# Optimization experiments

Hardware: AMD Instinct MI355X
Metric: run time of the kernel (lower is better)

The kernel has to match this reference:

```python
import jax, jax.numpy as jnp
import numpy as np

D_MODEL = 1024
N_HEAD = 16
DK = D_MODEL // N_HEAD
NEG = -10000.0  # module uses masked_fill with -10000.0, not -inf


def setup_inputs() -> dict:
    key = jax.random.key(0)
    k1, k2, k3 = jax.random.split(key, 3)
    B, T = 8, 1024
    x = jax.random.normal(k1, (B, T, D_MODEL), dtype=jnp.float32)
    # torch Linear(d, 3d, bias=False): y = x @ W.T with W [3d, d]; store transposed
    w_qkv = jax.random.normal(k2, (D_MODEL, 3 * D_MODEL), dtype=jnp.float32) * (1.0 / np.sqrt(D_MODEL))
    w_proj = jax.random.normal(k3, (D_MODEL, D_MODEL), dtype=jnp.float32) * (1.0 / np.sqrt(D_MODEL))
    return {"x": x, "w_qkv": w_qkv, "w_proj": w_proj}


def reference(x, w_qkv, w_proj):
    B, T, C = x.shape
    qkv = x @ w_qkv  # [B, T, 3C]
    q, k, v = jnp.split(qkv, 3, axis=-1)
    # [B, H, T, dk]
    q = q.reshape(B, T, N_HEAD, DK).transpose(0, 2, 1, 3)
    k = k.reshape(B, T, N_HEAD, DK).transpose(0, 2, 1, 3)
    v = v.reshape(B, T, N_HEAD, DK).transpose(0, 2, 1, 3)
    att = jnp.einsum('bhqd,bhkd->bhqk', q, k) / jnp.sqrt(jnp.float32(DK))
    causal = jnp.tril(jnp.ones((T, T), dtype=bool))  # [T, T]
    att = jnp.where(causal[None, None], att, NEG)
    att = jax.nn.softmax(att, axis=-1)
    y = jnp.einsum('bhqk,bhkd->bhqd', att, v)  # [B, H, T, dk]
    y = y.transpose(0, 2, 1, 3).reshape(B, T, C)
    return y @ w_proj
```

## Files before the change

kernel.cpp:

```cpp
#include <hip/hip_runtime.h>

typedef short bf16x8 __attribute__((ext_vector_type(8)));
typedef float f32x4 __attribute__((ext_vector_type(4)));

__device__ __forceinline__ unsigned short f2bf(float f) {
  unsigned u = __builtin_bit_cast(unsigned, f);
  u += 0x7fff + ((u >> 16) & 1);
  return (unsigned short)(u >> 16);
}

__device__ __forceinline__ void gload_lds16(const void* g, void* l) {
  __builtin_amdgcn_global_load_lds(
      (const __attribute__((address_space(1))) void*)g,
      (__attribute__((address_space(3))) void*)l, 16, 0, 0);
}

__global__ __launch_bounds__(256) void cvt_f32_bf16(const float* __restrict__ in,
                                                    unsigned short* __restrict__ out,
                                                    int n4) {
  int i = blockIdx.x * blockDim.x + threadIdx.x;
  int stride = gridDim.x * blockDim.x;
  for (; i < n4; i += stride) {
    float4 v = ((const float4*)in)[i];
    ushort4 o;
    o.x = f2bf(v.x); o.y = f2bf(v.y); o.z = f2bf(v.z); o.w = f2bf(v.w);
    ((ushort4*)out)[i] = o;
  }
}

__global__ __launch_bounds__(256) void tconv(const float* __restrict__ in,
                                             unsigned short* __restrict__ out,
                                             int R, int C) {
  __shared__ float tile[32][33];
  const int c0 = blockIdx.x * 32, r0 = blockIdx.y * 32;
  const int tid = threadIdx.x;
  const int tr = tid >> 3;
  const int tc4 = tid & 7;
  float4 v = *(const float4*)&in[(size_t)(r0 + tr) * C + c0 + tc4 * 4];
  tile[tr][tc4 * 4 + 0] = v.x;
  tile[tr][tc4 * 4 + 1] = v.y;
  tile[tr][tc4 * 4 + 2] = v.z;
  tile[tr][tc4 * 4 + 3] = v.w;
  __syncthreads();
#pragma unroll
  for (int i = 0; i < 4; ++i)
    out[(size_t)(c0 + tr) * R + r0 + tc4 * 4 + i] = f2bf(tile[tc4 * 4 + i][tr]);
}

__global__ __launch_bounds__(256) void transpV(const unsigned short* __restrict__ qkv,
                                               unsigned short* __restrict__ vT) {
  const int tt = blockIdx.x, bh = blockIdx.y;
  const int b = bh >> 4, h = bh & 15;
  __shared__ unsigned short tile[64 * 64];
  const int tid = threadIdx.x;
  const size_t gbase = (size_t)b * 1024 * 3072 + 2048 + (size_t)h * 64;
#pragma unroll
  for (int i = 0; i < 2; ++i) {
    int c = i * 256 + tid;
    int trow = c >> 3, dc = c & 7;
    *(uint4*)(&tile[c * 8]) =
        *(const uint4*)(qkv + gbase + (size_t)(tt * 64 + trow) * 3072 + dc * 8);
  }
  __syncthreads();
  const int d = tid & 63, th = tid >> 6;
  unsigned short buf[16];
#pragma unroll
  for (int j = 0; j < 16; ++j) buf[j] = tile[(th * 16 + j) * 64 + d];
  size_t obase = ((size_t)bh * 64 + d) * 1024 + tt * 64 + th * 16;
  *(uint4*)(&vT[obase]) = *(uint4*)(&buf[0]);
  *(uint4*)(&vT[obase + 8]) = *(uint4*)(&buf[8]);
}

template <int OUT_BF16>
__global__ __launch_bounds__(256) void gemm_bt(const unsigned short* __restrict__ A,
                                               const unsigned short* __restrict__ B,
                                               void* __restrict__ Cv,
                                               int M, int N, int K, int lda) {
  __shared__ unsigned short As[128 * 64];
  __shared__ unsigned short Bs[128 * 64];
  const int tid = threadIdx.x;
  const int wv = tid >> 6, lane = tid & 63;
  const int l15 = lane & 15, lg = lane >> 4;
  const int bm = blockIdx.y, bn = blockIdx.x;
  const int wr = wv >> 1, wc = wv & 1;
  f32x4 acc[4][4] = {};
  const unsigned short* Ab = A + (size_t)bm * 128 * lda;
  const unsigned short* Bb = B + (size_t)bn * 128 * K;

  for (int k0 = 0; k0 < K; k0 += 64) {
#pragma unroll
    for (int i = 0; i < 4; ++i) {
      int s = i * 256 + wv * 64 + lane;
      int row = s >> 3, pc = s & 7;
      int lc = pc ^ (row & 7);
      gload_lds16(Ab + (size_t)row * lda + k0 + lc * 8,
                  (char*)As + (size_t)(i * 256 + wv * 64) * 16);
      gload_lds16(Bb + (size_t)row * K + k0 + lc * 8,
                  (char*)Bs + (size_t)(i * 256 + wv * 64) * 16);
    }
    __syncthreads();
#pragma unroll
    for (int kh = 0; kh < 2; ++kh) {
      bf16x8 af[4], bf[4];
#pragma unroll
      for (int m = 0; m < 4; ++m) {
        int row = wr * 64 + m * 16 + l15;
        int pc = (kh * 4 + lg) ^ (row & 7);
        af[m] = *(const bf16x8*)((const char*)As + (row * 8 + pc) * 16);
      }
#pragma unroll
      for (int n = 0; n < 4; ++n) {
        int row = wc * 64 + n * 16 + l15;
        int pc = (kh * 4 + lg) ^ (row & 7);
        bf[n] = *(const bf16x8*)((const char*)Bs + (row * 8 + pc) * 16);
      }
#pragma unroll
      for (int m = 0; m < 4; ++m)
#pragma unroll
        for (int n = 0; n < 4; ++n)
          acc[m][n] = __builtin_amdgcn_mfma_f32_16x16x32_bf16(af[m], bf[n], acc[m][n], 0, 0, 0);
    }
    __syncthreads();
  }

  const int rbase = bm * 128 + wr * 64;
  const int cbase = bn * 128 + wc * 64;
#pragma unroll
  for (int m = 0; m < 4; ++m)
#pragma unroll
    for (int n = 0; n < 4; ++n)
#pragma unroll
      for (int r = 0; r < 4; ++r) {
        int row = rbase + m * 16 + lg * 4 + r;
        int col = cbase + n * 16 + l15;
        float v = acc[m][n][r];
        if (OUT_BF16)
          ((unsigned short*)Cv)[(size_t)row * N + col] = f2bf(v);
        else
          ((float*)Cv)[(size_t)row * N + col] = v;
      }
}

__global__ __launch_bounds__(256) void attn_fwd(const unsigned short* __restrict__ qkv,
                                                const unsigned short* __restrict__ vT,
                                                unsigned short* __restrict__ qkv_y) {
  const int pair = blockIdx.x;
  const int bh = blockIdx.y;
  const int b = bh >> 4, h = bh & 15;
  const int tid = threadIdx.x;
  const int wv = tid >> 6, lane = tid & 63;
  const int l15 = lane & 15, lg = lane >> 4;

  __shared__ unsigned short Ks[2][64 * 64];
  __shared__ unsigned short Vs[2][64 * 64];
  __shared__ unsigned short Ps[4][16][72];

  const size_t base = (size_t)b * 1024 * 3072;
  const float LOG2E = 1.44269504089f;

#pragma unroll
  for (int phase = 0; phase < 2; ++phase) {
    const int qt = phase ? 15 - pair : pair;
    const int q0 = qt * 64;
    const int qrow = q0 + wv * 16 + l15;
    const int rowg_base = q0 + wv * 16 + lg * 4;

    bf16x8 qa[2];
#pragma unroll
    for (int kh = 0; kh < 2; ++kh)
      qa[kh] = *(const bf16x8*)(qkv + base + (size_t)qrow * 3072 + h * 64 + kh * 32 + lg * 8);

    float m_r[4], l_r[4];
#pragma unroll
    for (int r = 0; r < 4; ++r) { m_r[r] = -1e30f; l_r[r] = 0.f; }
    f32x4 oacc[4] = {};

#pragma unroll
    for (int i = 0; i < 2; ++i) {
      int s = i * 256 + wv * 64 + lane;
      int row = s >> 3, pc = s & 7;
      int lc = pc ^ (row & 7);
      gload_lds16(qkv + base + (size_t)row * 3072 + 1024 + h * 64 + lc * 8,
                  (char*)(&Ks[0][0]) + (size_t)s * 16);
      gload_lds16(vT + ((size_t)bh * 64 + row) * 1024 + lc * 8,
                  (char*)(&Vs[0][0]) + (size_t)s * 16);
    }
    __syncthreads();

    for (int t = 0; t <= qt; ++t) {
      const int cur = t & 1;
      if (t < qt) {
        const int kv1 = (t + 1) * 64;
#pragma unroll
        for (int i = 0; i < 2; ++i) {
          int s = i * 256 + wv * 64 + lane;
          int row = s >> 3, pc = s & 7;
          int lc = pc ^ (row & 7);
          gload_lds16(qkv + base + (size_t)(kv1 + row) * 3072 + 1024 + h * 64 + lc * 8,
                      (char*)(&Ks[cur ^ 1][0]) + (size_t)s * 16);
          gload_lds16(vT + ((size_t)bh * 64 + row) * 1024 + kv1 + lc * 8,
                      (char*)(&Vs[cur ^ 1][0]) + (size_t)s * 16);
        }
      }

      const int kv0 = t * 64;
      f32x4 sacc[4] = {};
#pragma unroll
      for (int kh = 0; kh < 2; ++kh) {
        bf16x8 kf[4];
#pragma unroll
        for (int nt = 0; nt < 4; ++nt) {
          int row = nt * 16 + l15;
          int pc = (kh * 4 + lg) ^ (row & 7);
          kf[nt] = *(const bf16x8*)((const char*)(&Ks[cur][0]) + (row * 8 + pc) * 16);
        }
#pragma unroll
        for (int nt = 0; nt < 4; ++nt)
          sacc[nt] = __builtin_amdgcn_mfma_f32_16x16x32_bf16(qa[kh], kf[nt], sacc[nt], 0, 0, 0);
      }

      const bool diag = (t == qt);
      float sv[4][4];
#pragma unroll
      for (int nt = 0; nt < 4; ++nt)
#pragma unroll
        for (int r = 0; r < 4; ++r) {
          float s = sacc[nt][r] * 0.125f;
          if (diag && (kv0 + nt * 16 + l15 > rowg_base + r)) s = -1e30f;
          sv[nt][r] = s;
        }

#pragma unroll
      for (int r = 0; r < 4; ++r) {
        float tm = fmaxf(fmaxf(sv[0][r], sv[1][r]), fmaxf(sv[2][r], sv[3][r]));
        tm = fmaxf(tm, __shfl_xor(tm, 1));
        tm = fmaxf(tm, __shfl_xor(tm, 2));
        tm = fmaxf(tm, __shfl_xor(tm, 4));
        tm = fmaxf(tm, __shfl_xor(tm, 8));
        float mnew = fmaxf(m_r[r], tm);
        float sc2 = exp2f((m_r[r] - mnew) * LOG2E);
        m_r[r] = mnew;
        float ps = 0.f;
#pragma unroll
        for (int nt = 0; nt < 4; ++nt) {
          float p = exp2f((sv[nt][r] - mnew) * LOG2E);
          sv[nt][r] = p;
          ps += p;
        }
        ps += __shfl_xor(ps, 1);
        ps += __shfl_xor(ps, 2);
        ps += __shfl_xor(ps, 4);
        ps += __shfl_xor(ps, 8);
        l_r[r] = l_r[r] * sc2 + ps;
#pragma unroll
        for (int nt = 0; nt < 4; ++nt) oacc[nt][r] *= sc2;
      }

#pragma unroll
      for (int nt = 0; nt < 4; ++nt)
#pragma unroll
        for (int r = 0; r < 4; ++r)
          Ps[wv][lg * 4 + r][nt * 16 + l15] = f2bf(sv[nt][r]);

      bf16x8 pa[2];
#pragma unroll
      for (int kh = 0; kh < 2; ++kh)
        pa[kh] = *(const bf16x8*)&Ps[wv][l15][kh * 32 + lg * 8];

#pragma unroll
      for (int kh = 0; kh < 2; ++kh)
#pragma unroll
        for (int nt = 0; nt < 4; ++nt) {
          int row = nt * 16 + l15;
          int pc = (kh * 4 + lg) ^ (row & 7);
          bf16x8 vf = *(const bf16x8*)((const char*)(&Vs[cur][0]) + (row * 8 + pc) * 16);
          oacc[nt] = __builtin_amdgcn_mfma_f32_16x16x32_bf16(pa[kh], vf, oacc[nt], 0, 0, 0);
        }
      __syncthreads();
    }

#pragma unroll
    for (int nt = 0; nt < 4; ++nt)
#pragma unroll
      for (int r = 0; r < 4; ++r) {
        int row = rowg_base + r;
        int col = h * 64 + nt * 16 + l15;
        qkv_y[((size_t)b * 1024 + row) * 3072 + 2048 + col] = f2bf(oacc[nt][r] / l_r[r]);
      }
    __syncthreads();
  }
}

extern "C" void kernel_launch(void* const* d_in, const int* in_sizes, int n_in,
                              void* d_out, int out_size, void* d_ws, size_t ws_size,
                              hipStream_t stream) {
  const float* x = (const float*)d_in[0];
  const float* w_qkv = (const float*)d_in[1];
  const float* w_proj = (const float*)d_in[2];

  unsigned short* xb     = (unsigned short*)d_ws;
  unsigned short* vT     = (unsigned short*)d_ws;
  unsigned short* wqkvT  = (unsigned short*)((char*)d_ws + (16u << 20));
  unsigned short* wprojT = (unsigned short*)((char*)d_ws + (22u << 20));
  unsigned short* qkvb   = (unsigned short*)((char*)d_ws + (24u << 20));

  cvt_f32_bf16<<<2048, 256, 0, stream>>>(x, xb, (8 * 1024 * 1024) / 4);
  tconv<<<dim3(96, 32), 256, 0, stream>>>(w_qkv, wqkvT, 1024, 3072);
  tconv<<<dim3(32, 32), 256, 0, stream>>>(w_proj, wprojT, 1024, 1024);

  gemm_bt<1><<<dim3(24, 64), 256, 0, stream>>>(xb, wqkvT, qkvb, 8192, 3072, 1024, 1024);

  transpV<<<dim3(16, 128), 256, 0, stream>>>(qkvb, vT);

  attn_fwd<<<dim3(8, 128), 256, 0, stream>>>(qkvb, vT, qkvb);

  gemm_bt<0><<<dim3(8, 64), 256, 0, stream>>>(qkvb + 2048, wprojT, d_out, 8192, 1024, 1024, 3072);
}
```

Baseline: 271.8 us.

## Replace GEMM with 256x256 8-wave kernel using 4-stage LDS pipeline

Swaps the 128x128 single-buffered GEMM for a 256x256-tile, 512-thread kernel. It runs a 4-slot LDS ring with prefetch three K-steps ahead, split into two half-phases that overlap loads with MFMA, and adds setprio hints and an XCD-aware block swizzle. The goal is to hide global-load latency, raise data reuse per tile and improve L2 locality for both projection GEMMs. In exchange it uses more registers and LDS (one block per CU), and the output projection grid drops to 128 blocks, which may underfill the 256 CUs.

```diff
diff --git a/kernel.cpp b/kernel.cpp
--- a/kernel.cpp
+++ b/kernel.cpp
@@ -72,61 +72,104 @@
 }
 
 template <int OUT_BF16>
-__global__ __launch_bounds__(256) void gemm_bt(const unsigned short* __restrict__ A,
-                                               const unsigned short* __restrict__ B,
-                                               void* __restrict__ Cv,
-                                               int M, int N, int K, int lda) {
-  __shared__ unsigned short As[128 * 64];
-  __shared__ unsigned short Bs[128 * 64];
+__global__ __launch_bounds__(512, 1) void gemm8p(const unsigned short* __restrict__ A,
+                                                 const unsigned short* __restrict__ B,
+                                                 void* __restrict__ Cv,
+                                                 int M, int N, int K, int lda) {
+  __shared__ unsigned short As[4][256 * 32];
+  __shared__ unsigned short Bs[4][256 * 32];
   const int tid = threadIdx.x;
   const int wv = tid >> 6, lane = tid & 63;
+  const int wr = wv >> 2, wc = wv & 3;
   const int l15 = lane & 15, lg = lane >> 4;
-  const int bm = blockIdx.y, bn = blockIdx.x;
-  const int wr = wv >> 1, wc = wv & 1;
-  f32x4 acc[4][4] = {};
-  const unsigned short* Ab = A + (size_t)bm * 128 * lda;
-  const unsigned short* Bb = B + (size_t)bn * 128 * K;
-
-  for (int k0 = 0; k0 < K; k0 += 64) {
-#pragma unroll
-    for (int i = 0; i < 4; ++i) {
-      int s = i * 256 + wv * 64 + lane;
-      int row = s >> 3, pc = s & 7;
-      int lc = pc ^ (row & 7);
-      gload_lds16(Ab + (size_t)row * lda + k0 + lc * 8,
-                  (char*)As + (size_t)(i * 256 + wv * 64) * 16);
-      gload_lds16(Bb + (size_t)row * K + k0 + lc * 8,
-                  (char*)Bs + (size_t)(i * 256 + wv * 64) * 16);
-    }
-    __syncthreads();
-#pragma unroll
-    for (int kh = 0; kh < 2; ++kh) {
-      bf16x8 af[4], bf[4];
-#pragma unroll
-      for (int m = 0; m < 4; ++m) {
-        int row = wr * 64 + m * 16 + l15;
-        int pc = (kh * 4 + lg) ^ (row & 7);
-        af[m] = *(const bf16x8*)((const char*)As + (row * 8 + pc) * 16);
-      }
-#pragma unroll
-      for (int n = 0; n < 4; ++n) {
-        int row = wc * 64 + n * 16 + l15;
-        int pc = (kh * 4 + lg) ^ (row & 7);
-        bf[n] = *(const bf16x8*)((const char*)Bs + (row * 8 + pc) * 16);
-      }
-#pragma unroll
-      for (int m = 0; m < 4; ++m)
-#pragma unroll
-        for (int n = 0; n < 4; ++n)
-          acc[m][n] = __builtin_amdgcn_mfma_f32_16x16x32_bf16(af[m], bf[n], acc[m][n], 0, 0, 0);
-    }
-    __syncthreads();
+  const int srow = lane >> 2, schunk = lane & 3;
+
+  const int nbn = N >> 8;
+  const int nwg = (M >> 8) * nbn;
+  const int q8 = nwg >> 3;
+  const int lin = blockIdx.x;
+  const int swz = (lin & 7) * q8 + (lin >> 3);
+  const int bm = swz / nbn, bn = swz % nbn;
+
+  const unsigned short* Ab = A + (size_t)bm * 256 * lda;
+  const unsigned short* Bb = B + (size_t)bn * 256 * K;
+  const int NT = K >> 5;
+
+  auto STAGE = [&](int t, int p) {
+    int tt = t < NT ? t : NT - 1;
+    int slot = tt & 3;
+    int r = p * 128 + wv * 16 + srow;
+    int gc = (schunk ^ ((r >> 1) & 3)) * 8;
+    gload_lds16(Ab + (size_t)r * lda + tt * 32 + gc,
+                (char*)(&As[slot][0]) + (size_t)(p * 128 + wv * 16) * 64);
+    gload_lds16(Bb + (size_t)r * K + tt * 32 + gc,
+                (char*)(&Bs[slot][0]) + (size_t)(p * 128 + wv * 16) * 64);
+  };
+
+  f32x4 acc[8][4] = {};
+
+  STAGE(0, 0); STAGE(0, 1);
+  STAGE(1, 0); STAGE(1, 1);
+  STAGE(2, 0); STAGE(2, 1);
+  asm volatile("s_waitcnt vmcnt(8)" ::: "memory");
+  __builtin_amdgcn_s_barrier();
+  __builtin_amdgcn_sched_barrier(0);
+
+  for (int t = 0; t < NT; ++t) {
+    const int slot = t & 3;
+    const unsigned short* as = &As[slot][0];
+    const unsigned short* bs = &Bs[slot][0];
+    bf16x8 af[4], bf[4];
+
+#pragma unroll
+    for (int n = 0; n < 4; ++n) {
+      int r = wc * 64 + n * 16 + l15;
+      bf[n] = *(const bf16x8*)(bs + r * 32 + (lg ^ ((r >> 1) & 3)) * 8);
+    }
+#pragma unroll
+    for (int m = 0; m < 4; ++m) {
+      int r = wr * 128 + m * 16 + l15;
+      af[m] = *(const bf16x8*)(as + r * 32 + (lg ^ ((r >> 1) & 3)) * 8);
+    }
+    STAGE(t + 3, 0);
+    __builtin_amdgcn_s_barrier();
+    __builtin_amdgcn_sched_barrier(0);
+    __builtin_amdgcn_s_setprio(1);
+#pragma unroll
+    for (int m = 0; m < 4; ++m)
+#pragma unroll
+      for (int n = 0; n < 4; ++n)
+        acc[m][n] = __builtin_amdgcn_mfma_f32_16x16x32_bf16(af[m], bf[n], acc[m][n], 0, 0, 0);
+    __builtin_amdgcn_s_setprio(0);
+    __builtin_amdgcn_s_barrier();
+    __builtin_amdgcn_sched_barrier(0);
+
+#pragma unroll
+    for (int m = 0; m < 4; ++m) {
+      int r = wr * 128 + (m + 4) * 16 + l15;
+      af[m] = *(const bf16x8*)(as + r * 32 + (lg ^ ((r >> 1) & 3)) * 8);
+    }
+    STAGE(t + 3, 1);
+    asm volatile("s_waitcnt vmcnt(8)" ::: "memory");
+    __builtin_amdgcn_s_barrier();
+    __builtin_amdgcn_sched_barrier(0);
+    __builtin_amdgcn_s_setprio(1);
+#pragma unroll
+    for (int m = 0; m < 4; ++m)
+#pragma unroll
+      for (int n = 0; n < 4; ++n)
+        acc[m + 4][n] = __builtin_amdgcn_mfma_f32_16x16x32_bf16(af[m], bf[n], acc[m + 4][n], 0, 0, 0);
+    __builtin_amdgcn_s_setprio(0);
+    __builtin_amdgcn_s_barrier();
+    __builtin_amdgcn_sched_barrier(0);
   }
 
-  const int rbase = bm * 128 + wr * 64;
-  const int cbase = bn * 128 + wc * 64;
-#pragma unroll
-  for (int m = 0; m < 4; ++m)
+  asm volatile("s_waitcnt vmcnt(0)" ::: "memory");
+
+  const int rbase = bm * 256 + wr * 128;
+  const int cbase = bn * 256 + wc * 64;
+#pragma unroll
+  for (int m = 0; m < 8; ++m)
 #pragma unroll
     for (int n = 0; n < 4; ++n)
 #pragma unroll
@@ -308,11 +351,11 @@
   tconv<<<dim3(96, 32), 256, 0, stream>>>(w_qkv, wqkvT, 1024, 3072);
   tconv<<<dim3(32, 32), 256, 0, stream>>>(w_proj, wprojT, 1024, 1024);
 
-  gemm_bt<1><<<dim3(24, 64), 256, 0, stream>>>(xb, wqkvT, qkvb, 8192, 3072, 1024, 1024);
+  gemm8p<1><<<384, 512, 0, stream>>>(xb, wqkvT, qkvb, 8192, 3072, 1024, 1024);
 
   transpV<<<dim3(16, 128), 256, 0, stream>>>(qkvb, vT);
 
   attn_fwd<<<dim3(8, 128), 256, 0, stream>>>(qkvb, vT, qkvb);
 
-  gemm_bt<0><<<dim3(8, 64), 256, 0, stream>>>(qkvb + 2048, wprojT, d_out, 8192, 1024, 1024, 3072);
-}
+  gemm8p<0><<<128, 512, 0, stream>>>(qkvb + 2048, wprojT, d_out, 8192, 1024, 1024, 3072);
+}
```

Result: slower. 288.8 us (+6.2%).
